# Optimization experiments

Hardware: AMD Instinct MI355X
Metric: run time of the kernel (lower is better)

The kernel has to match this reference:

```python
import jax, jax.numpy as jnp
import numpy as np

EPS = 1e-12


def setup_inputs() -> dict:
    key = jax.random.key(0)
    n, k, Eu, iterations = 200_000, 7, 1_600_000, 3
    k1, k2, k3 = jax.random.split(key, 3)
    # undirected edge list; each undirected edge yields two directed edges
    su = jax.random.randint(k1, (Eu,), 0, n, dtype=jnp.int32)
    du = jax.random.randint(k2, (Eu,), 0, n, dtype=jnp.int32)
    src = jnp.concatenate([su, du])                                   # [E]
    dst = jnp.concatenate([du, su])                                   # [E]
    rev = jnp.concatenate([jnp.arange(Eu, 2 * Eu, dtype=jnp.int32),
                           jnp.arange(Eu, dtype=jnp.int32)])          # [E]
    # node priors (rows sum to 1), mimicking the soft label priors
    prior = jax.random.uniform(k3, (n, k), minval=0.1, maxval=1.0)
    prior = prior / prior.sum(axis=1, keepdims=True)
    # label-to-label potential: log(beta) on the diagonal (beta = 3.0)
    W = jnp.log(3.0) * jnp.eye(k, dtype=jnp.float32)
    return {"prior": prior, "W": W, "src": src, "dst": dst,
            "rev": rev, "iterations": iterations}


def reference(prior, W, src, dst, rev, iterations):
    n, k = prior.shape
    E = src.shape[0]
    psi = jnp.exp(jnp.clip(W, -10.0, 10.0))                           # [k,k]
    msgs = jnp.full((E, k), 1.0 / k, dtype=prior.dtype)

    def step(msgs, _):
        # product of incoming messages per node, in log-space (msgs >= EPS)
        logm = jnp.log(msgs)                                          # [E,k]
        logP = jax.ops.segment_sum(logm, dst, num_segments=n)         # [n,k]
        # per directed edge (i -> j): remove reverse message j -> i
        prod_in_i = jnp.exp(logP[src] - logm[rev])                    # [E,k]
        b = jnp.maximum(prior[src] * prod_in_i, EPS)                  # [E,k]
        m_new = jnp.maximum(b @ psi, EPS)                             # [E,k]
        m_new = m_new / jnp.maximum(m_new.sum(-1, keepdims=True), EPS)
        return m_new, None

    msgs, _ = jax.lax.scan(step, msgs, None, length=int(iterations))

    # beliefs
    logP = jax.ops.segment_sum(jnp.log(msgs), dst, num_segments=n)    # [n,k]
    b = jnp.maximum(prior * jnp.exp(logP), EPS)
    return b / jnp.maximum(b.sum(-1, keepdims=True), EPS)
```

## Files before the change

### kernel.cpp

```cpp
#include <hip/hip_runtime.h>
#include <hip/hip_bf16.h>
#include <hip/hip_fp16.h>

#define K 7
#define EPSF 1e-12f
#define LOG_INV_K (-1.9459101090932196f)
#define LOG7 1.9459101090932196f
#define LOG2_EPS (-39.8631371f)
#define LN2 0.69314718056f
#define INV_LN2 1.44269504f
#define SBN 512
#define SBSH 9
#define NSBMAX 768
#define PB 256

__device__ __forceinline__ float ldf(const void* p, size_t idx, int mode) {
    return mode ? ((const float*)p)[idx]
                : __bfloat162float(((const __hip_bfloat16*)p)[idx]);
}

__device__ __forceinline__ void load_psi(const void* W, float* psi, int mode) {
    if (threadIdx.x < K * K) {
        float w = ldf(W, threadIdx.x, mode);
        w = fminf(fmaxf(w, -10.f), 10.f);
        psi[threadIdx.x] = __expf(w);
    }
    __syncthreads();
}

__device__ __forceinline__ void bp_lin(const float* b, const float* psi, float* m) {
    float o[K], sum = 0.f;
#pragma unroll
    for (int j = 0; j < K; j++) {
        float acc = 0.f;
#pragma unroll
        for (int i = 0; i < K; i++) acc += b[i] * psi[i * K + j];
        o[j] = fmaxf(acc, EPSF);
        sum += o[j];
    }
    float inv = __fdividef(1.f, fmaxf(sum, EPSF));
#pragma unroll
    for (int j = 0; j < K; j++) m[j] = o[j] * inv;
}

__device__ __forceinline__ void acc_log_msg(const float* b, const float* psi, float* acc) {
    float m[K];
    bp_lin(b, psi, m);
#pragma unroll
    for (int j = 0; j < K; j++) acc[j] += __logf(m[j]);
}

__device__ __forceinline__ void dec_pd(uint4 w, float* p, int* degv, int* u1) {
    p[0] = __uint_as_float((w.x & 0xffffu) << 16);
    p[1] = __uint_as_float(w.x & 0xffff0000u);
    p[2] = __uint_as_float((w.y & 0xffffu) << 16);
    p[3] = __uint_as_float(w.y & 0xffff0000u);
    p[4] = __uint_as_float((w.z & 0xffffu) << 16);
    p[5] = __uint_as_float(w.z & 0xffff0000u);
    p[6] = __uint_as_float((w.w & 0xffffu) << 16);
    *degv = (int)((w.w >> 16) & 0x7fffu);
    *u1 = (int)(w.w >> 31);
}

__device__ __forceinline__ unsigned short f2h(float f) {
    __half h = __float2half_rn(f);
    return *reinterpret_cast<unsigned short*>(&h);
}
__device__ __forceinline__ float h2f(unsigned short u) {
    __half h;
    *reinterpret_cast<unsigned short*>(&h) = u;
    return __half2float(h);
}
__device__ __forceinline__ uint4 pack7h(const float* m, int E) {
    uint4 r;
    r.x = (unsigned)f2h(m[0]) | ((unsigned)f2h(m[1]) << 16);
    r.y = (unsigned)f2h(m[2]) | ((unsigned)f2h(m[3]) << 16);
    r.z = (unsigned)f2h(m[4]) | ((unsigned)f2h(m[5]) << 16);
    r.w = (unsigned)f2h(m[6]) | ((unsigned)(E & 0xffff) << 16);
    return r;
}
__device__ __forceinline__ int unpack7h(uint4 w, float* m) {
    m[0] = h2f((unsigned short)(w.x & 0xffffu));
    m[1] = h2f((unsigned short)(w.x >> 16));
    m[2] = h2f((unsigned short)(w.y & 0xffffu));
    m[3] = h2f((unsigned short)(w.y >> 16));
    m[4] = h2f((unsigned short)(w.z & 0xffffu));
    m[5] = h2f((unsigned short)(w.z >> 16));
    m[6] = h2f((unsigned short)(w.w & 0xffffu));
    return (int)(short)(w.w >> 16);
}

__global__ void sniff11_kernel(const void* __restrict__ W, int* __restrict__ prm,
                               int* __restrict__ btot, int NSB) {
    if (blockIdx.x != 0) return;
    for (int i = threadIdx.x; i < NSB; i += 64) btot[i] = 0;
    if (threadIdx.x != 0) return;
    const unsigned int* Wraw = (const unsigned int*)W;
    int mode = ((Wraw[0] >> 16) != 0u) ? 1 : 0;
    float diag0 = 0.f, offd0 = 0.f;
    int structured = 1;
    for (int i = 0; i < K; i++)
        for (int j = 0; j < K; j++) {
            float w = ldf(W, i * K + j, mode);
            w = fminf(fmaxf(w, -10.f), 10.f);
            float e = __expf(w);
            if (i == 0 && j == 0) diag0 = e;
            if (i == 0 && j == 1) offd0 = e;
            if (i == j) { if (i > 0 && e != diag0) structured = 0; }
            else       { if (!(i == 0 && j == 1) && e != offd0) structured = 0; }
        }
    if (!(offd0 >= 0.2f) || !(diag0 >= offd0)) structured = 0;
    prm[0] = mode | (structured << 1);
    ((float*)prm)[1] = offd0;
    ((float*)prm)[2] = diag0;
}

__global__ void hist6_kernel(const int* __restrict__ dst, int* __restrict__ hist,
                             int* __restrict__ btot, int E, int EPB, int NSB) {
    __shared__ int h[NSBMAX];
    for (int i = threadIdx.x; i < NSB; i += 256) h[i] = 0;
    __syncthreads();
    int blk = blockIdx.x;
    int e0 = blk * EPB, e1 = min(e0 + EPB, E);
    for (int e = e0 + (int)threadIdx.x; e < e1; e += 256)
        atomicAdd(&h[dst[e] >> SBSH], 1);
    __syncthreads();
    for (int i = threadIdx.x; i < NSB; i += 256) {
        int c = h[i];
        hist[i * PB + blk] = c;
        if (c) atomicAdd(&btot[i], c);
    }
}

__global__ void bscan6_kernel(const int* __restrict__ btot, int* __restrict__ boff, int NSB) {
    __shared__ int s[1024];
    int t = threadIdx.x;
    int x = (t < NSB) ? btot[t] : 0;
    s[t] = x;
    __syncthreads();
    for (int o = 1; o < 1024; o <<= 1) {
        int y = (t >= o) ? s[t - o] : 0;
        __syncthreads();
        s[t] += y;
        __syncthreads();
    }
    if (t < NSB) boff[t] = s[t] - x;
    if (t == NSB - 1) boff[NSB] = s[t];
}

__global__ void sscan6_kernel(const int* __restrict__ hist, const int* __restrict__ boff,
                              int* __restrict__ woff) {
    __shared__ int s[PB];
    int b = blockIdx.x, t = threadIdx.x;
    int x = hist[b * PB + t];
    s[t] = x;
    __syncthreads();
    for (int o = 1; o < PB; o <<= 1) {
        int y = (t >= o) ? s[t - o] : 0;
        __syncthreads();
        s[t] += y;
        __syncthreads();
    }
    woff[b * PB + t] = boff[b] + s[t] - x;
}

__global__ void part6_kernel(const int* __restrict__ src, const int* __restrict__ dst,
                             const int* __restrict__ woff, unsigned int* __restrict__ coarse,
                             int E, int EPB, int NSB) {
    __shared__ int cur[NSBMAX];
    int blk = blockIdx.x;
    for (int i = threadIdx.x; i < NSB; i += 256) cur[i] = woff[i * PB + blk];
    __syncthreads();
    int e0 = blk * EPB, e1 = min(e0 + EPB, E);
    for (int e = e0 + (int)threadIdx.x; e < e1; e += 256) {
        int d = dst[e];
        int b = d >> SBSH;
        unsigned int pk = (unsigned int)src[e] | ((unsigned int)(d & (SBN - 1)) << 18);
        int pos = atomicAdd(&cur[b], 1);
        coarse[pos] = pk;
    }
}

__global__ void cfill9_kernel(const unsigned int* __restrict__ coarse,
                              const int* __restrict__ boff,
                              const void* __restrict__ prior, const int* __restrict__ prm,
                              int* __restrict__ cur, int* __restrict__ nbr,
                              uint4* __restrict__ PD, int n) {
    __shared__ int lcnt[SBN], lcur[SBN];
    int b = blockIdx.x, t = threadIdx.x;
    int mode = prm[0] & 1;
    for (int i = t; i < SBN; i += 256) lcnt[i] = 0;
    __syncthreads();
    int s0 = boff[b], s1 = boff[b + 1];
    for (int i = s0 + t; i < s1; i += 256)
        atomicAdd(&lcnt[coarse[i] >> 18], 1);
    __syncthreads();
    if (t == 0) {
        int a = s0;
        for (int l = 0; l < SBN; l++) { lcur[l] = a; a += lcnt[l]; }
    }
    __syncthreads();
    int v0 = b << SBSH;
    for (int i = t; i < SBN; i += 256) {
        int v = v0 + i;
        if (v >= n) continue;
        int degv = lcnt[i];
        cur[v] = lcur[i] + degv;
        unsigned int pb[K];
        float p[K];
        if (mode == 0) {
            const unsigned short* pr = (const unsigned short*)prior;
#pragma unroll
            for (int j = 0; j < K; j++) {
                pb[j] = pr[(size_t)v * K + j];
                p[j] = __uint_as_float(pb[j] << 16);
            }
        } else {
            const float* pr = (const float*)prior;
#pragma unroll
            for (int j = 0; j < K; j++) {
                p[j] = pr[(size_t)v * K + j];
                __hip_bfloat16 hh = __float2bfloat16(p[j]);
                pb[j] = *(unsigned short*)&hh;
            }
        }
        float es = __expf((float)(degv - 1) * LOG_INV_K);
        float mx = p[0];
#pragma unroll
        for (int j = 1; j < K; j++) mx = fmaxf(mx, p[j]);
        unsigned int u1 = (mx * es <= EPSF) ? 1u : 0u;
        int dcap = degv > 0x7fff ? 0x7fff : degv;
        uint4 w;
        w.x = pb[0] | (pb[1] << 16);
        w.y = pb[2] | (pb[3] << 16);
        w.z = pb[4] | (pb[5] << 16);
        w.w = pb[6] | (((unsigned int)dcap) << 16) | (u1 << 31);
        PD[v] = w;
    }
    __syncthreads();
    for (int i = s0 + t; i < s1; i += 256) {
        unsigned int w = coarse[i];
        int pos = atomicAdd(&lcur[w >> 18], 1);
        nbr[pos] = (int)(w & 0x3FFFFu);
    }
}

__global__ void mbuild11_kernel(const uint4* __restrict__ PD, const void* __restrict__ W,
                                const int* __restrict__ prm, uint4* __restrict__ M1h, int n) {
    __shared__ float psi[K * K];
    int pm = prm[0];
    int mode = pm & 1, strq = (pm >> 1) & 1;
    float offd = ((const float*)prm)[1], diag = ((const float*)prm)[2];
    load_psi(W, psi, mode);
    int v = blockIdx.x * blockDim.x + threadIdx.x;
    if (v >= n) return;
    float p[K]; int dv, u1v;
    dec_pd(PD[v], p, &dv, &u1v);
    float es = __expf((float)(dv - 1) * LOG_INV_K);
    float b[K], S = 0.f;
#pragma unroll
    for (int i = 0; i < K; i++) { b[i] = fmaxf(p[i] * es, EPSF); S += b[i]; }
    float m1n[K];
    if (strq) {
        float cb = diag - offd, norm = 6.f * offd + diag;
        float sc = __fdividef(7.f, S * norm);
#pragma unroll
        for (int i = 0; i < K; i++) m1n[i] = (offd * S + cb * b[i]) * sc;
    } else {
        float m1[K];
        bp_lin(b, psi, m1);
#pragma unroll
        for (int i = 0; i < K; i++) m1n[i] = 7.f * m1[i];
    }
    M1h[v] = pack7h(m1n, 0);
}

__global__ void n2v11_kernel(const int* __restrict__ cur, const int* __restrict__ nbr,
                             const uint4* __restrict__ M1h, const uint4* __restrict__ PD,
                             const int* __restrict__ prm, uint4* __restrict__ LP1, int n) {
    int t = blockIdx.x * blockDim.x + threadIdx.x;
    int v = t >> 2, qi = t & 3;
    if (v >= n) return;
    int start = v ? cur[v - 1] : 0, end = cur[v];
    int len = end - start;
    int lo = start + ((len * qi) >> 2), hi = start + ((len * (qi + 1)) >> 2);
    float acc[K] = {1.f, 1.f, 1.f, 1.f, 1.f, 1.f, 1.f};
    int e = lo;
    for (; e + 3 < hi; e += 4) {
        int u0 = nbr[e], u1 = nbr[e + 1], u2 = nbr[e + 2], u3 = nbr[e + 3];
        uint4 w0 = M1h[u0], w1 = M1h[u1], w2 = M1h[u2], w3 = M1h[u3];
        float a[K], b[K], c[K], d[K];
        unpack7h(w0, a); unpack7h(w1, b); unpack7h(w2, c); unpack7h(w3, d);
#pragma unroll
        for (int i = 0; i < K; i++) acc[i] *= (a[i] * b[i]) * (c[i] * d[i]);
    }
    for (; e < hi; e++) {
        float a[K];
        unpack7h(M1h[nbr[e]], a);
#pragma unroll
        for (int i = 0; i < K; i++) acc[i] *= fmaxf(a[i], 1e-30f);
    }
#pragma unroll
    for (int i = 0; i < K; i++) {
        acc[i] *= __shfl_xor(acc[i], 1, 64);
        acc[i] *= __shfl_xor(acc[i], 2, 64);
    }
    if (qi) return;
    float pv[K]; int dv, u1v;
    dec_pd(PD[v], pv, &dv, &u1v);
    float le[K], mx = -1e30f;
    float corr = (float)len * LOG7;
#pragma unroll
    for (int i = 0; i < K; i++) {
        le[i] = __logf(fmaxf(pv[i] * acc[i], 1e-37f)) - corr;
        mx = fmaxf(mx, le[i]);
    }
    int E1 = (int)ceilf(mx * INV_LN2);
    float fm[K];
#pragma unroll
    for (int i = 0; i < K; i++) fm[i] = __expf(le[i] - (float)E1 * LN2);
    LP1[v] = pack7h(fm, E1);
}

__global__ void n3v11_kernel(const int* __restrict__ cur, const int* __restrict__ nbr,
                             const uint4* __restrict__ PD, const uint4* __restrict__ LP1,
                             const void* __restrict__ W, const int* __restrict__ prm,
                             uint4* __restrict__ Q2h, int n) {
    __shared__ float psi[K * K];
    int pm = prm[0];
    int mode = pm & 1, strq = (pm >> 1) & 1;
    float offd = ((const float*)prm)[1], diag = ((const float*)prm)[2];
    load_psi(W, psi, mode);
    int t = blockIdx.x * blockDim.x + threadIdx.x;
    int v = t >> 2, qi = t & 3;
    if (v >= n) return;
    int start = v ? cur[v - 1] : 0, end = cur[v];
    int len = end - start;
    int lo = start + ((len * qi) >> 2), hi = start + ((len * (qi + 1)) >> 2);
    float cb = diag - offd, norm = 6.f * offd + diag;
    float pv[K]; int dv, u1v;
    dec_pd(PD[v], pv, &dv, &u1v);
    float rm1v[K], mrv = 0.f;
    if (strq && u1v) {
#pragma unroll
        for (int i = 0; i < K; i++) rm1v[i] = 7.f;
        mrv = 7.f;
    } else {
        float es = __expf((float)(dv - 1) * LOG_INV_K);
        float b1[K], S1 = 0.f;
#pragma unroll
        for (int i = 0; i < K; i++) { b1[i] = fmaxf(pv[i] * es, EPSF); S1 += b1[i]; }
        if (strq) {
            float inv = __fdividef(1.f, S1 * norm);
#pragma unroll
            for (int i = 0; i < K; i++) {
                float m1 = (offd * S1 + cb * b1[i]) * inv;
                rm1v[i] = __fdividef(1.f, m1);
                mrv = fmaxf(mrv, rm1v[i]);
            }
        } else {
            float m1[K];
            bp_lin(b1, psi, m1);
#pragma unroll
            for (int i = 0; i < K; i++) rm1v[i] = __fdividef(1.f, m1[i]);
        }
    }
    float acc[K];
    int cn = 0;
    if (strq) {
        int Ethr = (int)floorf(LOG2_EPS - log2f(mrv));
#pragma unroll
        for (int i = 0; i < K; i++) acc[i] = 1.f;
        auto proc = [&](uint4 q) {
            float m[K];
            int E = unpack7h(q, m);
            if (E <= Ethr) return;
            float b[K], S = 0.f;
#pragma unroll
            for (int i = 0; i < K; i++) {
                b[i] = fmaxf(ldexpf(m[i] * rm1v[i], E), EPSF);
                S += b[i];
            }
            float crS = __fdividef(cb, S);
#pragma unroll
            for (int i = 0; i < K; i++) acc[i] *= fmaf(crS, b[i], offd);
            cn++;
        };
        int e = lo;
        for (; e + 3 < hi; e += 4) {
            int u0 = nbr[e], u1 = nbr[e + 1], u2 = nbr[e + 2], u3 = nbr[e + 3];
            uint4 q0 = LP1[u0], q1 = LP1[u1], q2 = LP1[u2], q3 = LP1[u3];
            proc(q0); proc(q1); proc(q2); proc(q3);
        }
        for (; e < hi; e++) proc(LP1[nbr[e]]);
#pragma unroll
        for (int i = 0; i < K; i++) {
            acc[i] *= __shfl_xor(acc[i], 1, 64);
            acc[i] *= __shfl_xor(acc[i], 2, 64);
        }
    } else {
#pragma unroll
        for (int i = 0; i < K; i++) acc[i] = 0.f;
        for (int e = lo; e < hi; e++) {
            float m[K];
            int E = unpack7h(LP1[nbr[e]], m);
            float b[K];
#pragma unroll
            for (int i = 0; i < K; i++)
                b[i] = fmaxf(ldexpf(m[i] * rm1v[i], E), EPSF);
            acc_log_msg(b, psi, acc);
        }
#pragma unroll
        for (int i = 0; i < K; i++) {
            acc[i] += __shfl_xor(acc[i], 1, 64);
            acc[i] += __shfl_xor(acc[i], 2, 64);
        }
    }
    cn += __shfl_xor(cn, 1, 64);
    cn += __shfl_xor(cn, 2, 64);
    if (qi) return;
    float le2[K], mx = -1e30f;
    if (strq) {
        float corr = (float)cn * __logf(norm) + (float)(len - cn) * LOG7;
#pragma unroll
        for (int i = 0; i < K; i++) {
            le2[i] = __logf(fmaxf(pv[i] * acc[i], 1e-37f)) - corr;
            mx = fmaxf(mx, le2[i]);
        }
    } else {
#pragma unroll
        for (int i = 0; i < K; i++) {
            le2[i] = __logf(fmaxf(pv[i], 1e-37f)) + acc[i];
            mx = fmaxf(mx, le2[i]);
        }
    }
    int E2 = (int)ceilf(mx * INV_LN2);
    float fm[K];
#pragma unroll
    for (int i = 0; i < K; i++) fm[i] = __expf(le2[i] - (float)E2 * LN2);
    Q2h[v] = pack7h(fm, E2);
}

__global__ void n4v11_kernel(const int* __restrict__ cur, const int* __restrict__ nbr,
                             const uint4* __restrict__ M1h, const uint4* __restrict__ Q2h,
                             const uint4* __restrict__ LP1, const void* __restrict__ prior,
                             const void* __restrict__ W, const int* __restrict__ prm,
                             void* __restrict__ out, int n) {
    __shared__ float psi[K * K];
    int pm = prm[0];
    int mode = pm & 1, strq = (pm >> 1) & 1;
    float offd = ((const float*)prm)[1], diag = ((const float*)prm)[2];
    load_psi(W, psi, mode);
    int t = blockIdx.x * blockDim.x + threadIdx.x;
    int v = t >> 2, qi = t & 3;
    if (v >= n) return;
    int start = v ? cur[v - 1] : 0, end = cur[v];
    int len = end - start;
    int lo = start + ((len * qi) >> 2), hi = start + ((len * (qi + 1)) >> 2);
    float cb = diag - offd, norm = 6.f * offd + diag;
    float e1v[K];
    {
        float m[K];
        int E1 = unpack7h(LP1[v], m);
#pragma unroll
        for (int i = 0; i < K; i++) e1v[i] = ldexpf(m[i], E1);
    }
    float acc[K];
    int cn = 0;
    if (strq) {
        float mx1 = e1v[0];
#pragma unroll
        for (int i = 1; i < K; i++) mx1 = fmaxf(mx1, e1v[i]);
        float F = __fdividef(norm, offd) * 1.01f;
        int m2u = (F * mx1 <= EPSF);
        int Ethr2 = (int)floorf(LOG2_EPS - log2f(7.f));
        int Ethr3 = (int)floorf(LOG2_EPS - log2f(F));
#pragma unroll
        for (int i = 0; i < K; i++) acc[i] = 1.f;
        if (m2u) {
            auto proc = [&](uint4 q) {
                float m[K];
                int E2 = unpack7h(q, m);
                if (E2 <= Ethr2) return;
                float b3[K], S = 0.f;
#pragma unroll
                for (int i = 0; i < K; i++) {
                    b3[i] = fmaxf(ldexpf(m[i] * 7.f, E2), EPSF);
                    S += b3[i];
                }
                float crS = __fdividef(cb, S);
#pragma unroll
                for (int i = 0; i < K; i++) acc[i] *= fmaf(crS, b3[i], offd);
                cn++;
            };
            int e = lo;
            for (; e + 3 < hi; e += 4) {
                int u0 = nbr[e], u1 = nbr[e + 1], u2 = nbr[e + 2], u3 = nbr[e + 3];
                uint4 q0 = Q2h[u0], q1 = Q2h[u1], q2 = Q2h[u2], q3 = Q2h[u3];
                proc(q0); proc(q1); proc(q2); proc(q3);
            }
            for (; e < hi; e++) proc(Q2h[nbr[e]]);
        } else {
            for (int e = lo; e < hi; e++) {
                int u = nbr[e];
                uint4 q = Q2h[u];
                float m[K];
                int E2 = unpack7h(q, m);
                if (E2 <= Ethr3) continue;
                float tt[K];
                unpack7h(M1h[u], tt);
                float b2[K], S2 = 0.f;
#pragma unroll
                for (int i = 0; i < K; i++) {
                    b2[i] = fmaxf(e1v[i] * __fdividef(7.f, tt[i]), EPSF);
                    S2 += b2[i];
                }
                float inv2 = __fdividef(1.f, S2 * norm);
                float b3[K], S3 = 0.f;
#pragma unroll
                for (int i = 0; i < K; i++) {
                    float m2v = (offd * S2 + cb * b2[i]) * inv2;
                    float e2 = ldexpf(m[i], E2);
                    b3[i] = fmaxf(__fdividef(e2, m2v), EPSF);
                    S3 += b3[i];
                }
                float crS3 = __fdividef(cb, S3);
#pragma unroll
                for (int i = 0; i < K; i++) acc[i] *= fmaf(crS3, b3[i], offd);
                cn++;
            }
        }
#pragma unroll
        for (int i = 0; i < K; i++) {
            acc[i] *= __shfl_xor(acc[i], 1, 64);
            acc[i] *= __shfl_xor(acc[i], 2, 64);
        }
    } else {
#pragma unroll
        for (int i = 0; i < K; i++) acc[i] = 0.f;
        for (int e = lo; e < hi; e++) {
            int u = nbr[e];
            uint4 q = Q2h[u];
            float m[K];
            int E2 = unpack7h(q, m);
            float tt[K];
            unpack7h(M1h[u], tt);
            float b2[K];
#pragma unroll
            for (int i = 0; i < K; i++)
                b2[i] = fmaxf(e1v[i] * __fdividef(7.f, fmaxf(tt[i], 1e-30f)), EPSF);
            float m2[K];
            bp_lin(b2, psi, m2);
            float b3[K];
#pragma unroll
            for (int i = 0; i < K; i++) {
                float e2 = ldexpf(m[i], E2);
                b3[i] = fmaxf(__fdividef(e2, m2[i]), EPSF);
            }
            acc_log_msg(b3, psi, acc);
        }
#pragma unroll
        for (int i = 0; i < K; i++) {
            acc[i] += __shfl_xor(acc[i], 1, 64);
            acc[i] += __shfl_xor(acc[i], 2, 64);
        }
    }
    cn += __shfl_xor(cn, 1, 64);
    cn += __shfl_xor(cn, 2, 64);
    if (qi) return;
    float bb[K], sum = 0.f;
    if (strq) {
        float corr = (float)cn * __logf(norm) + (float)(len - cn) * LOG7;
#pragma unroll
        for (int i = 0; i < K; i++) {
            float p = ldf(prior, (size_t)v * K + i, mode);
            bb[i] = fmaxf(__expf(__logf(fmaxf(p * acc[i], 1e-37f)) - corr), EPSF);
            sum += bb[i];
        }
    } else {
#pragma unroll
        for (int i = 0; i < K; i++) {
            float p = ldf(prior, (size_t)v * K + i, mode);
            bb[i] = fmaxf(p * __expf(acc[i]), EPSF);
            sum += bb[i];
        }
    }
    float inv = __fdividef(1.f, fmaxf(sum, EPSF));
#pragma unroll
    for (int i = 0; i < K; i++) {
        float val = bb[i] * inv;
        if (mode) ((float*)out)[(size_t)v * K + i] = val;
        else ((__hip_bfloat16*)out)[(size_t)v * K + i] = __float2bfloat16(val);
    }
}

__device__ __forceinline__ void bp_msg(const float* b, const float* psi, float* lm) {
    float m[K];
    bp_lin(b, psi, m);
#pragma unroll
    for (int j = 0; j < K; j++) lm[j] = __logf(m[j]);
}
__device__ __forceinline__ void msg1(const void* prior, int node, int degv, int mode,
                                     const float* psi, float* lm) {
    float es = __expf((float)(degv - 1) * LOG_INV_K);
    float b[K];
#pragma unroll
    for (int i = 0; i < K; i++)
        b[i] = fmaxf(ldf(prior, (size_t)node * K + i, mode) * es, EPSF);
    bp_msg(b, psi, lm);
}
__device__ __forceinline__ void msgF(const void* prior, int node,
                                     const float* __restrict__ logP,
                                     const float* lmrev, int mode,
                                     const float* psi, float* lm) {
    float b[K];
#pragma unroll
    for (int i = 0; i < K; i++)
        b[i] = fmaxf(ldf(prior, (size_t)node * K + i, mode) *
                     __expf(logP[(size_t)node * K + i] - lmrev[i]), EPSF);
    bp_msg(b, psi, lm);
}
__global__ void deg_kernel(const int* __restrict__ su, const int* __restrict__ du,
                           int* __restrict__ deg, int Eu) {
    int u = blockIdx.x * blockDim.x + threadIdx.x;
    if (u >= Eu) return;
    atomicAdd(&deg[su[u]], 1);
    atomicAdd(&deg[du[u]], 1);
}
__global__ void pass1_kernel(const int* __restrict__ su, const int* __restrict__ du,
                             const int* __restrict__ deg, const void* __restrict__ prior,
                             const void* __restrict__ W, const int* __restrict__ prm,
                             float* __restrict__ logP1, int Eu) {
    __shared__ float psi[K * K];
    int mode = prm[0] & 1;
    load_psi(W, psi, mode);
    int u = blockIdx.x * blockDim.x + threadIdx.x;
    if (u >= Eu) return;
    int s = su[u], d = du[u];
    float lm[K];
    msg1(prior, s, deg[s], mode, psi, lm);
#pragma unroll
    for (int j = 0; j < K; j++) atomicAdd(&logP1[(size_t)d * K + j], lm[j]);
    msg1(prior, d, deg[d], mode, psi, lm);
#pragma unroll
    for (int j = 0; j < K; j++) atomicAdd(&logP1[(size_t)s * K + j], lm[j]);
}
__global__ void pass2_kernel(const int* __restrict__ su, const int* __restrict__ du,
                             const int* __restrict__ deg, const void* __restrict__ prior,
                             const void* __restrict__ W, const int* __restrict__ prm,
                             const float* __restrict__ logP1, float* __restrict__ logP2, int Eu) {
    __shared__ float psi[K * K];
    int mode = prm[0] & 1;
    load_psi(W, psi, mode);
    int u = blockIdx.x * blockDim.x + threadIdx.x;
    if (u >= Eu) return;
    int s = su[u], d = du[u];
    float lm1sd[K], lm1ds[K], lm[K];
    msg1(prior, s, deg[s], mode, psi, lm1sd);
    msg1(prior, d, deg[d], mode, psi, lm1ds);
    msgF(prior, s, logP1, lm1ds, mode, psi, lm);
#pragma unroll
    for (int j = 0; j < K; j++) atomicAdd(&logP2[(size_t)d * K + j], lm[j]);
    msgF(prior, d, logP1, lm1sd, mode, psi, lm);
#pragma unroll
    for (int j = 0; j < K; j++) atomicAdd(&logP2[(size_t)s * K + j], lm[j]);
}
__global__ void pass3_kernel(const int* __restrict__ su, const int* __restrict__ du,
                             const int* __restrict__ deg, const void* __restrict__ prior,
                             const void* __restrict__ W, const int* __restrict__ prm,
                             const float* __restrict__ logP1, const float* __restrict__ logP2,
                             float* __restrict__ logP3, int Eu) {
    __shared__ float psi[K * K];
    int mode = prm[0] & 1;
    load_psi(W, psi, mode);
    int u = blockIdx.x * blockDim.x + threadIdx.x;
    if (u >= Eu) return;
    int s = su[u], d = du[u];
    float lm1sd[K], lm1ds[K], lm2sd[K], lm2ds[K], lm[K];
    msg1(prior, s, deg[s], mode, psi, lm1sd);
    msg1(prior, d, deg[d], mode, psi, lm1ds);
    msgF(prior, s, logP1, lm1ds, mode, psi, lm2sd);
    msgF(prior, d, logP1, lm1sd, mode, psi, lm2ds);
    msgF(prior, s, logP2, lm2ds, mode, psi, lm);
#pragma unroll
    for (int j = 0; j < K; j++) atomicAdd(&logP3[(size_t)d * K + j], lm[j]);
    msgF(prior, d, logP2, lm2sd, mode, psi, lm);
#pragma unroll
    for (int j = 0; j < K; j++) atomicAdd(&logP3[(size_t)s * K + j], lm[j]);
}
__global__ void belief_kernel(const float* __restrict__ logP3, const void* __restrict__ prior,
                              const int* __restrict__ prm, void* __restrict__ out, int n) {
    int v = blockIdx.x * blockDim.x + threadIdx.x;
    if (v >= n) return;
    int mode = prm[0] & 1;
    float b[K], sum = 0.f;
#pragma unroll
    for (int j = 0; j < K; j++) {
        b[j] = fmaxf(ldf(prior, (size_t)v * K + j, mode) * __expf(logP3[(size_t)v * K + j]), EPSF);
        sum += b[j];
    }
    float inv = __fdividef(1.f, fmaxf(sum, EPSF));
#pragma unroll
    for (int j = 0; j < K; j++) {
        float val = b[j] * inv;
        if (mode) ((float*)out)[(size_t)v * K + j] = val;
        else ((__hip_bfloat16*)out)[(size_t)v * K + j] = __float2bfloat16(val);
    }
}

extern "C" void kernel_launch(void* const* d_in, const int* in_sizes, int n_in,
                              void* d_out, int out_size, void* d_ws, size_t ws_size,
                              hipStream_t stream) {
    const void* prior = d_in[0];
    const void* W     = d_in[1];
    const int* src = (const int*)d_in[2];
    const int* dst = (const int*)d_in[3];

    int n  = in_sizes[0] / K;
    int E  = in_sizes[2];
    int Eu = E / 2;

    const int B = 256;
    int gn  = (n + B - 1) / B;
    int gn4 = (4 * n + B - 1) / B;
    int ge  = (Eu + B - 1) / B;

    int NSB = (n + SBN - 1) >> SBSH;
    int EPB = (E + PB - 1) / PB;

    char* ws = (char*)d_ws;
    size_t off = 0;
    auto alloc = [&](size_t bytes) { size_t o = off; off = (off + bytes + 127) & ~(size_t)127; return o; };

    size_t xsz = (size_t)E * 4;
    if ((size_t)n * 48 > xsz) xsz = (size_t)n * 48;
    size_t o_nbr  = alloc((size_t)E * 4);
    size_t o_X    = alloc(xsz);
    size_t o_PD   = alloc((size_t)n * 16);
    size_t o_cur  = alloc((size_t)n * 4);
    size_t o_hist = alloc((size_t)NSB * PB * 4);
    size_t o_woff = alloc((size_t)NSB * PB * 4);
    size_t o_boff = alloc((size_t)(NSB + 1) * 4);
    size_t o_btot = alloc((size_t)NSB * 4);
    size_t o_prm  = alloc(64);
    size_t need_v11 = off;

    bool v11_ok = (ws_size >= need_v11) && (n <= (1 << 18)) && (NSB <= NSBMAX) && (NSB >= 1);

    if (v11_ok) {
        int*   nbr    = (int*)(ws + o_nbr);
        unsigned int* coarse = (unsigned int*)(ws + o_X);
        uint4* LP1    = (uint4*)(ws + o_X);
        uint4* Q2h    = (uint4*)(ws + o_X + (size_t)n * 16);
        uint4* M1h    = (uint4*)(ws + o_X + (size_t)n * 32);
        uint4* PD     = (uint4*)(ws + o_PD);
        int*   cur    = (int*)(ws + o_cur);
        int*   hist   = (int*)(ws + o_hist);
        int*   woff   = (int*)(ws + o_woff);
        int*   boff   = (int*)(ws + o_boff);
        int*   btot   = (int*)(ws + o_btot);
        int*   prm    = (int*)(ws + o_prm);

        sniff11_kernel<<<1, 64, 0, stream>>>(W, prm, btot, NSB);
        hist6_kernel<<<PB, B, 0, stream>>>(dst, hist, btot, E, EPB, NSB);
        bscan6_kernel<<<1, 1024, 0, stream>>>(btot, boff, NSB);
        sscan6_kernel<<<NSB, PB, 0, stream>>>(hist, boff, woff);
        part6_kernel<<<PB, B, 0, stream>>>(src, dst, woff, coarse, E, EPB, NSB);
        cfill9_kernel<<<NSB, B, 0, stream>>>(coarse, boff, prior, prm, cur, nbr, PD, n);
        mbuild11_kernel<<<gn, B, 0, stream>>>(PD, W, prm, M1h, n);
        n2v11_kernel<<<gn4, B, 0, stream>>>(cur, nbr, M1h, PD, prm, LP1, n);
        n3v11_kernel<<<gn4, B, 0, stream>>>(cur, nbr, PD, LP1, W, prm, Q2h, n);
        n4v11_kernel<<<gn4, B, 0, stream>>>(cur, nbr, M1h, Q2h, LP1, prior, W, prm, d_out, n);
        return;
    }

    {
        float* logP1 = (float*)d_ws;
        float* logP2 = logP1 + (size_t)n * K;
        float* logP3 = logP2 + (size_t)n * K;
        int*   deg   = (int*)(logP3 + (size_t)n * K);
        int*   prm   = deg + n;
        int*   btot  = prm + 8;
        sniff11_kernel<<<1, 64, 0, stream>>>(W, prm, btot, 0);
        hipMemsetAsync(d_ws, 0, ((size_t)3 * n * K + n) * sizeof(float), stream);
        deg_kernel<<<ge, B, 0, stream>>>(src, dst, deg, Eu);
        pass1_kernel<<<ge, B, 0, stream>>>(src, dst, deg, prior, W, prm, logP1, Eu);
        pass2_kernel<<<ge, B, 0, stream>>>(src, dst, deg, prior, W, prm, logP1, logP2, Eu);
        pass3_kernel<<<ge, B, 0, stream>>>(src, dst, deg, prior, W, prm, logP1, logP2, logP3, Eu);
        belief_kernel<<<gn, B, 0, stream>>>(logP3, prior, prm, d_out, n);
    }
}
```

Before: 294.2 us.

## Filter neighbors via compact byte exponent arrays before gathering full messages

```diff
diff --git a/kernel.cpp b/kernel.cpp
--- a/kernel.cpp
+++ b/kernel.cpp
@@ -13,6 +13,7 @@
 #define SBSH 9
 #define NSBMAX 768
 #define PB 256
+#define CAP 16
 
 __device__ __forceinline__ float ldf(const void* p, size_t idx, int mode) {
     return mode ? ((const float*)p)[idx]
@@ -88,6 +89,9 @@
     m[5] = h2f((unsigned short)(w.z >> 16));
     m[6] = h2f((unsigned short)(w.w & 0xffffu));
     return (int)(short)(w.w >> 16);
+}
+__device__ __forceinline__ signed char clampE(int E) {
+    return (signed char)(E < -120 ? -120 : (E > 120 ? 120 : E));
 }
 
 __global__ void sniff11_kernel(const void* __restrict__ W, int* __restrict__ prm,
@@ -275,9 +279,10 @@
     M1h[v] = pack7h(m1n, 0);
 }
 
-__global__ void n2v11_kernel(const int* __restrict__ cur, const int* __restrict__ nbr,
+__global__ void n2v12_kernel(const int* __restrict__ cur, const int* __restrict__ nbr,
                              const uint4* __restrict__ M1h, const uint4* __restrict__ PD,
-                             const int* __restrict__ prm, uint4* __restrict__ LP1, int n) {
+                             const int* __restrict__ prm, uint4* __restrict__ LP1,
+                             signed char* __restrict__ E1x, int n) {
     int t = blockIdx.x * blockDim.x + threadIdx.x;
     int v = t >> 2, qi = t & 3;
     if (v >= n) return;
@@ -320,13 +325,16 @@
 #pragma unroll
     for (int i = 0; i < K; i++) fm[i] = __expf(le[i] - (float)E1 * LN2);
     LP1[v] = pack7h(fm, E1);
-}
-
-__global__ void n3v11_kernel(const int* __restrict__ cur, const int* __restrict__ nbr,
+    E1x[v] = clampE(E1);
+}
+
+__global__ void n3v12_kernel(const int* __restrict__ cur, const int* __restrict__ nbr,
                              const uint4* __restrict__ PD, const uint4* __restrict__ LP1,
+                             const signed char* __restrict__ E1x,
                              const void* __restrict__ W, const int* __restrict__ prm,
-                             uint4* __restrict__ Q2h, int n) {
+                             uint4* __restrict__ Q2h, signed char* __restrict__ E2x, int n) {
     __shared__ float psi[K * K];
+    __shared__ int lively[256 * CAP];
     int pm = prm[0];
     int mode = pm & 1, strq = (pm >> 1) & 1;
     float offd = ((const float*)prm)[1], diag = ((const float*)prm)[2];
@@ -340,11 +348,10 @@
     float cb = diag - offd, norm = 6.f * offd + diag;
     float pv[K]; int dv, u1v;
     dec_pd(PD[v], pv, &dv, &u1v);
-    float rm1v[K], mrv = 0.f;
+    float rm1v[K];
     if (strq && u1v) {
 #pragma unroll
         for (int i = 0; i < K; i++) rm1v[i] = 7.f;
-        mrv = 7.f;
     } else {
         float es = __expf((float)(dv - 1) * LOG_INV_K);
         float b1[K], S1 = 0.f;
@@ -353,11 +360,8 @@
         if (strq) {
             float inv = __fdividef(1.f, S1 * norm);
 #pragma unroll
-            for (int i = 0; i < K; i++) {
-                float m1 = (offd * S1 + cb * b1[i]) * inv;
-                rm1v[i] = __fdividef(1.f, m1);
-                mrv = fmaxf(mrv, rm1v[i]);
-            }
+            for (int i = 0; i < K; i++)
+                rm1v[i] = __fdividef(1.f, (offd * S1 + cb * b1[i]) * inv);
         } else {
             float m1[K];
             bp_lin(b1, psi, m1);
@@ -368,13 +372,13 @@
     float acc[K];
     int cn = 0;
     if (strq) {
-        int Ethr = (int)floorf(LOG2_EPS - log2f(mrv));
+        float F = __fdividef(norm, offd) * 1.01f;
+        int Ethr = (int)floorf(LOG2_EPS - log2f(F));
 #pragma unroll
         for (int i = 0; i < K; i++) acc[i] = 1.f;
         auto proc = [&](uint4 q) {
             float m[K];
             int E = unpack7h(q, m);
-            if (E <= Ethr) return;
             float b[K], S = 0.f;
 #pragma unroll
             for (int i = 0; i < K; i++) {
@@ -386,13 +390,22 @@
             for (int i = 0; i < K; i++) acc[i] *= fmaf(crS, b[i], offd);
             cn++;
         };
+        int base = (int)threadIdx.x * CAP;
+        int cnt = 0;
+        auto consider = [&](int u, int Eu) {
+            if (Eu > Ethr) {
+                if (cnt < CAP) lively[base + cnt++] = u;
+                else proc(LP1[u]);
+            }
+        };
         int e = lo;
         for (; e + 3 < hi; e += 4) {
             int u0 = nbr[e], u1 = nbr[e + 1], u2 = nbr[e + 2], u3 = nbr[e + 3];
-            uint4 q0 = LP1[u0], q1 = LP1[u1], q2 = LP1[u2], q3 = LP1[u3];
-            proc(q0); proc(q1); proc(q2); proc(q3);
-        }
-        for (; e < hi; e++) proc(LP1[nbr[e]]);
+            int a0 = E1x[u0], a1 = E1x[u1], a2 = E1x[u2], a3 = E1x[u3];
+            consider(u0, a0); consider(u1, a1); consider(u2, a2); consider(u3, a3);
+        }
+        for (; e < hi; e++) { int u = nbr[e]; consider(u, (int)E1x[u]); }
+        for (int j = 0; j < cnt; j++) proc(LP1[lively[base + j]]);
 #pragma unroll
         for (int i = 0; i < K; i++) {
             acc[i] *= __shfl_xor(acc[i], 1, 64);
@@ -439,14 +452,17 @@
 #pragma unroll
     for (int i = 0; i < K; i++) fm[i] = __expf(le2[i] - (float)E2 * LN2);
     Q2h[v] = pack7h(fm, E2);
-}
-
-__global__ void n4v11_kernel(const int* __restrict__ cur, const int* __restrict__ nbr,
+    E2x[v] = clampE(E2);
+}
+
+__global__ void n4v12_kernel(const int* __restrict__ cur, const int* __restrict__ nbr,
                              const uint4* __restrict__ M1h, const uint4* __restrict__ Q2h,
+                             const signed char* __restrict__ E2x,
                              const uint4* __restrict__ LP1, const void* __restrict__ prior,
                              const void* __restrict__ W, const int* __restrict__ prm,
                              void* __restrict__ out, int n) {
     __shared__ float psi[K * K];
+    __shared__ int lively[256 * CAP];
     int pm = prm[0];
     int mode = pm & 1, strq = (pm >> 1) & 1;
     float offd = ((const float*)prm)[1], diag = ((const float*)prm)[2];
@@ -473,63 +489,65 @@
         for (int i = 1; i < K; i++) mx1 = fmaxf(mx1, e1v[i]);
         float F = __fdividef(norm, offd) * 1.01f;
         int m2u = (F * mx1 <= EPSF);
-        int Ethr2 = (int)floorf(LOG2_EPS - log2f(7.f));
-        int Ethr3 = (int)floorf(LOG2_EPS - log2f(F));
+        int Ethr = (int)floorf(LOG2_EPS - log2f(F));
 #pragma unroll
         for (int i = 0; i < K; i++) acc[i] = 1.f;
-        if (m2u) {
-            auto proc = [&](uint4 q) {
-                float m[K];
-                int E2 = unpack7h(q, m);
-                if (E2 <= Ethr2) return;
-                float b3[K], S = 0.f;
-#pragma unroll
-                for (int i = 0; i < K; i++) {
-                    b3[i] = fmaxf(ldexpf(m[i] * 7.f, E2), EPSF);
-                    S += b3[i];
-                }
-                float crS = __fdividef(cb, S);
-#pragma unroll
-                for (int i = 0; i < K; i++) acc[i] *= fmaf(crS, b3[i], offd);
-                cn++;
-            };
-            int e = lo;
-            for (; e + 3 < hi; e += 4) {
-                int u0 = nbr[e], u1 = nbr[e + 1], u2 = nbr[e + 2], u3 = nbr[e + 3];
-                uint4 q0 = Q2h[u0], q1 = Q2h[u1], q2 = Q2h[u2], q3 = Q2h[u3];
-                proc(q0); proc(q1); proc(q2); proc(q3);
+        auto proc2u = [&](int u) {
+            float m[K];
+            int E2 = unpack7h(Q2h[u], m);
+            float b3[K], S = 0.f;
+#pragma unroll
+            for (int i = 0; i < K; i++) {
+                b3[i] = fmaxf(ldexpf(m[i] * 7.f, E2), EPSF);
+                S += b3[i];
             }
-            for (; e < hi; e++) proc(Q2h[nbr[e]]);
-        } else {
-            for (int e = lo; e < hi; e++) {
-                int u = nbr[e];
-                uint4 q = Q2h[u];
-                float m[K];
-                int E2 = unpack7h(q, m);
-                if (E2 <= Ethr3) continue;
-                float tt[K];
-                unpack7h(M1h[u], tt);
-                float b2[K], S2 = 0.f;
-#pragma unroll
-                for (int i = 0; i < K; i++) {
-                    b2[i] = fmaxf(e1v[i] * __fdividef(7.f, tt[i]), EPSF);
-                    S2 += b2[i];
-                }
-                float inv2 = __fdividef(1.f, S2 * norm);
-                float b3[K], S3 = 0.f;
-#pragma unroll
-                for (int i = 0; i < K; i++) {
-                    float m2v = (offd * S2 + cb * b2[i]) * inv2;
-                    float e2 = ldexpf(m[i], E2);
-                    b3[i] = fmaxf(__fdividef(e2, m2v), EPSF);
-                    S3 += b3[i];
-                }
-                float crS3 = __fdividef(cb, S3);
-#pragma unroll
-                for (int i = 0; i < K; i++) acc[i] *= fmaf(crS3, b3[i], offd);
-                cn++;
+            float crS = __fdividef(cb, S);
+#pragma unroll
+            for (int i = 0; i < K; i++) acc[i] *= fmaf(crS, b3[i], offd);
+            cn++;
+        };
+        auto procGen = [&](int u) {
+            float m[K];
+            int E2 = unpack7h(Q2h[u], m);
+            float tt[K];
+            unpack7h(M1h[u], tt);
+            float b2[K], S2 = 0.f;
+#pragma unroll
+            for (int i = 0; i < K; i++) {
+                b2[i] = fmaxf(e1v[i] * __fdividef(7.f, tt[i]), EPSF);
+                S2 += b2[i];
             }
-        }
+            float inv2 = __fdividef(1.f, S2 * norm);
+            float b3[K], S3 = 0.f;
+#pragma unroll
+            for (int i = 0; i < K; i++) {
+                float m2v = (offd * S2 + cb * b2[i]) * inv2;
+                float e2 = ldexpf(m[i], E2);
+                b3[i] = fmaxf(__fdividef(e2, m2v), EPSF);
+                S3 += b3[i];
+            }
+            float crS3 = __fdividef(cb, S3);
+#pragma unroll
+            for (int i = 0; i < K; i++) acc[i] *= fmaf(crS3, b3[i], offd);
+            cn++;
+        };
+        int base = (int)threadIdx.x * CAP;
+        int cnt = 0;
+        auto consider = [&](int u, int Eu) {
+            if (Eu > Ethr) {
+                if (cnt < CAP) lively[base + cnt++] = u;
+                else { if (m2u) proc2u(u); else procGen(u); }
+            }
+        };
+        int e = lo;
+        for (; e + 3 < hi; e += 4) {
+            int u0 = nbr[e], u1 = nbr[e + 1], u2 = nbr[e + 2], u3 = nbr[e + 3];
+            int a0 = E2x[u0], a1 = E2x[u1], a2 = E2x[u2], a3 = E2x[u3];
+            consider(u0, a0); consider(u1, a1); consider(u2, a2); consider(u3, a3);
+        }
+        for (; e < hi; e++) { int u = nbr[e]; consider(u, (int)E2x[u]); }
+        if (m2u) { for (int j = 0; j < cnt; j++) proc2u(lively[base + j]); }
+        else     { for (int j = 0; j < cnt; j++) procGen(lively[base + j]); }
 #pragma unroll
         for (int i = 0; i < K; i++) {
             acc[i] *= __shfl_xor(acc[i], 1, 64);
@@ -737,23 +755,27 @@
     size_t o_nbr  = alloc((size_t)E * 4);
     size_t o_X    = alloc(xsz);
     size_t o_PD   = alloc((size_t)n * 16);
+    size_t o_E1x  = alloc((size_t)n);
+    size_t o_E2x  = alloc((size_t)n);
     size_t o_cur  = alloc((size_t)n * 4);
     size_t o_hist = alloc((size_t)NSB * PB * 4);
     size_t o_woff = alloc((size_t)NSB * PB * 4);
     size_t o_boff = alloc((size_t)(NSB + 1) * 4);
     size_t o_btot = alloc((size_t)NSB * 4);
     size_t o_prm  = alloc(64);
-    size_t need_v11 = off;
-
-    bool v11_ok = (ws_size >= need_v11) && (n <= (1 << 18)) && (NSB <= NSBMAX) && (NSB >= 1);
-
-    if (v11_ok) {
+    size_t need_v12 = off;
+
+    bool v12_ok = (ws_size >= need_v12) && (n <= (1 << 18)) && (NSB <= NSBMAX) && (NSB >= 1);
+
+    if (v12_ok) {
         int*   nbr    = (int*)(ws + o_nbr);
         unsigned int* coarse = (unsigned int*)(ws + o_X);
         uint4* LP1    = (uint4*)(ws + o_X);
         uint4* Q2h    = (uint4*)(ws + o_X + (size_t)n * 16);
         uint4* M1h    = (uint4*)(ws + o_X + (size_t)n * 32);
         uint4* PD     = (uint4*)(ws + o_PD);
+        signed char* E1x = (signed char*)(ws + o_E1x);
+        signed char* E2x = (signed char*)(ws + o_E2x);
         int*   cur    = (int*)(ws + o_cur);
         int*   hist   = (int*)(ws + o_hist);
         int*   woff   = (int*)(ws + o_woff);
@@ -768,9 +790,10 @@
         part6_kernel<<<PB, B, 0, stream>>>(src, dst, woff, coarse, E, EPB, NSB);
         cfill9_kernel<<<NSB, B, 0, stream>>>(coarse, boff, prior, prm, cur, nbr, PD, n);
         mbuild11_kernel<<<gn, B, 0, stream>>>(PD, W, prm, M1h, n);
-        n2v11_kernel<<<gn4, B, 0, stream>>>(cur, nbr, M1h, PD, prm, LP1, n);
-        n3v11_kernel<<<gn4, B, 0, stream>>>(cur, nbr, PD, LP1, W, prm, Q2h, n);
-        n4v11_kernel<<<gn4, B, 0, stream>>>(cur, nbr, M1h, Q2h, LP1, prior, W, prm, d_out, n);
+        n2v12_kernel<<<gn4, B, 0, stream>>>(cur, nbr, M1h, PD, prm, LP1, E1x, n);
+        n3v12_kernel<<<gn4, B, 0, stream>>>(cur, nbr, PD, LP1, E1x, W, prm, Q2h, E2x, n);
+        n4v12_kernel<<<gn4, B, 0, stream>>>(cur, nbr, M1h, Q2h, E2x, LP1, prior, W, prm,
+                                            d_out, n);
         return;
     }
 
```

After: 287.9 us. -2.2%, faster.
